# Kernel tuning notes

Hardware: AMD Instinct MI355X
Metric: run time of the kernel (lower is better)

The kernel has to match this reference:

```python
import jax, jax.numpy as jnp
import numpy as np

EMBED_DIM = 1024
NUM_HEADS = 16
D_K = EMBED_DIM // NUM_HEADS
B, T = 4, 2048


def setup_inputs() -> dict:
    key = jax.random.key(0)
    k_x, k_wqkv, k_wo = jax.random.split(key, 3)
    x = jax.random.normal(k_x, (B, T, EMBED_DIM), dtype=jnp.float32)
    # kaiming_normal on torch Linear weight [out,in]: std = sqrt(2/fan_in)=sqrt(2/embed_dim)
    std = np.sqrt(2.0 / EMBED_DIM).astype(np.float32)
    # store weights already transposed to [in, out] for y = x @ W + b
    W_qkv = jax.random.normal(k_wqkv, (EMBED_DIM, 3 * EMBED_DIM), dtype=jnp.float32) * std
    b_qkv = jnp.zeros((3 * EMBED_DIM,), dtype=jnp.float32)
    W_o = jax.random.normal(k_wo, (EMBED_DIM, EMBED_DIM), dtype=jnp.float32) * std
    b_o = jnp.zeros((EMBED_DIM,), dtype=jnp.float32)
    return {"x": x, "W_qkv": W_qkv, "b_qkv": b_qkv, "W_o": W_o, "b_o": b_o}


def reference(x, W_qkv, b_qkv, W_o, b_o):
    Bsz, Tlen, D = x.shape
    qkv = x @ W_qkv + b_qkv                      # [B,T,3D]
    q, k, v = jnp.split(qkv, 3, axis=-1)
    # split heads -> [B,H,T,d_k]
    def heads(t):
        return t.reshape(Bsz, Tlen, NUM_HEADS, D_K).transpose(0, 2, 1, 3)
    q, k, v = heads(q), heads(k), heads(v)
    scores = jnp.einsum('bhqd,bhkd->bhqk', q, k) / jnp.sqrt(jnp.float32(D_K))
    causal = jnp.tril(jnp.ones((Tlen, Tlen), dtype=bool))
    scores = jnp.where(causal[None, None], scores, -jnp.inf)
    attn = jax.nn.softmax(scores, axis=-1)
    out = jnp.einsum('bhqk,bhkd->bhqd', attn, v)  # [B,H,T,d_k]
    out = out.transpose(0, 2, 1, 3).reshape(Bsz, Tlen, D)
    return out @ W_o + b_o
```

## Files before the change

### kernel.cpp

```cpp
#include <hip/hip_runtime.h>
#include <hip/hip_bf16.h>
#include <math.h>

typedef unsigned short u16;
typedef __attribute__((ext_vector_type(8))) short bf16x8;
typedef __attribute__((ext_vector_type(4))) float f32x4;

#define BATCH 4
#define TSEQ  2048
#define HEADS 16
#define DK    64
#define EMB   1024
#define MROWS 8192
#define NQKV  3072
#define PHT   ((size_t)MROWS * EMB)

__device__ __forceinline__ u16 f2bf(float f) {
    union { float f; unsigned int i; } v;
    v.f = f;
    unsigned int x = v.i;
    return (u16)((x + 0x7FFFu + ((x >> 16) & 1u)) >> 16);
}

__device__ __forceinline__ unsigned int pk2bf(float a, float b) {
    float2 f2; f2.x = a; f2.y = b;
    union { __hip_bfloat162 h; unsigned int u; } cv;
    cv.h = __float22bfloat162_rn(f2);
    return cv.u;
}

__device__ __forceinline__ void gl2lds16(const u16* g, u16* l) {
    __builtin_amdgcn_global_load_lds(
        (const __attribute__((address_space(1))) unsigned int*)g,
        (__attribute__((address_space(3))) unsigned int*)l, 16, 0, 0);
}

__global__ __launch_bounds__(256) void convert_x(const float* __restrict__ X,
                                                 u16* __restrict__ Xb) {
    int i = (blockIdx.x * 256 + threadIdx.x) * 4;
    float4 v = *(const float4*)&X[i];
    ushort4 o;
    o.x = f2bf(v.x); o.y = f2bf(v.y); o.z = f2bf(v.z); o.w = f2bf(v.w);
    *(ushort4*)&Xb[i] = o;
}

__global__ __launch_bounds__(256) void transpose_both(const float* __restrict__ Wqkv,
                                                      const float* __restrict__ Wo,
                                                      u16* __restrict__ Wt,
                                                      u16* __restrict__ Wot) {
    __shared__ float tile[32][33];
    const int tx = threadIdx.x & 31, ty = threadIdx.x >> 5;
    const int K = 1024;
    const float* W;
    u16* D;
    int N, bx;
    if (blockIdx.x < 96) { W = Wqkv; D = Wt; N = 3072; bx = blockIdx.x; }
    else                 { W = Wo;   D = Wot; N = 1024; bx = blockIdx.x - 96; }
    const int by = blockIdx.y;
#pragma unroll
    for (int s = 0; s < 4; s++)
        tile[ty + 8 * s][tx] = W[(size_t)(by * 32 + ty + 8 * s) * N + bx * 32 + tx];
    __syncthreads();
#pragma unroll
    for (int s = 0; s < 4; s++)
        D[(size_t)(bx * 32 + ty + 8 * s) * K + by * 32 + tx] = f2bf(tile[tx][ty + 8 * s]);
}

template <int KDIM>
__device__ __forceinline__ void gemm_core256(const u16* __restrict__ A,
                                             const u16* __restrict__ Bt,
                                             u16* pool,
                                             int m0, int n0, int wm, int wn,
                                             int tid, int lo, int quad,
                                             f32x4 (&acc)[4][4]) {
    constexpr int NT = KDIM / 64;
    static_assert(NT >= 4 && (NT % 2) == 0, "NT even, >=4");

    const u16* ga[2];
    const u16* gb[4];
#pragma unroll
    for (int c = 0; c < 2; c++) {
        int chunk = c * 512 + tid, row = chunk >> 3, p = chunk & 7;
        ga[c] = A + (size_t)(m0 + row) * KDIM + (p ^ (row & 7)) * 8;
    }
#pragma unroll
    for (int c = 0; c < 4; c++) {
        int chunk = c * 512 + tid, row = chunk >> 3, p = chunk & 7;
        gb[c] = Bt + (size_t)(n0 + row) * KDIM + (p ^ (row & 7)) * 8;
    }

    auto stage = [&](int b) {
        u16* As = pool + b * 24576;
        u16* Bs = As + 8192;
#pragma unroll
        for (int c = 0; c < 2; c++) {
            gl2lds16(ga[c], As + (size_t)(c * 512 + tid) * 8);
            ga[c] += 64;
        }
#pragma unroll
        for (int c = 0; c < 4; c++) {
            gl2lds16(gb[c], Bs + (size_t)(c * 512 + tid) * 8);
            gb[c] += 64;
        }
    };

    bf16x8 afA[2][4], bwA[2][4], afB[2][4], bwB[2][4];

    auto ldfrag = [&](int b, bf16x8 (&af)[2][4], bf16x8 (&bw)[2][4]) {
        const u16* As = pool + b * 24576;
        const u16* Bs = As + 8192;
#pragma unroll
        for (int ks = 0; ks < 2; ks++) {
#pragma unroll
            for (int i = 0; i < 4; i++) {
                int r = wm + i * 16 + lo;
                af[ks][i] = *(const bf16x8*)&As[r * 64 + ((ks * 4 + quad) ^ (r & 7)) * 8];
            }
#pragma unroll
            for (int j = 0; j < 4; j++) {
                int r = wn + j * 16 + lo;
                bw[ks][j] = *(const bf16x8*)&Bs[r * 64 + ((ks * 4 + quad) ^ (r & 7)) * 8];
            }
        }
    };

    auto domfma = [&](bf16x8 (&af)[2][4], bf16x8 (&bw)[2][4]) {
        __builtin_amdgcn_sched_barrier(0);
        __builtin_amdgcn_s_setprio(1);
#pragma unroll
        for (int ks = 0; ks < 2; ks++)
#pragma unroll
            for (int i = 0; i < 4; i++)
#pragma unroll
                for (int j = 0; j < 4; j++)
                    acc[i][j] = __builtin_amdgcn_mfma_f32_16x16x32_bf16(
                        af[ks][i], bw[ks][j], acc[i][j], 0, 0, 0);
        __builtin_amdgcn_s_setprio(0);
    };

    stage(0); stage(1); stage(2);
    asm volatile("s_waitcnt vmcnt(12)" ::: "memory");
    __builtin_amdgcn_s_barrier();
    ldfrag(0, afA, bwA);

#pragma unroll
    for (int kt = 0; kt < NT; kt++) {
        if (kt < NT - 1) {
            asm volatile("s_waitcnt lgkmcnt(0)" ::: "memory");
            if (kt < NT - 2)
                asm volatile("s_waitcnt vmcnt(6)" ::: "memory");
            else
                asm volatile("s_waitcnt vmcnt(0)" ::: "memory");
            __builtin_amdgcn_s_barrier();
            if (kt + 3 < NT) stage(kt % 3);
            if (kt & 1) ldfrag((kt + 1) % 3, afA, bwA);
            else        ldfrag((kt + 1) % 3, afB, bwB);
        }
        if (kt & 1) domfma(afB, bwB);
        else        domfma(afA, bwA);
    }
}

__global__ __launch_bounds__(512, 1) void gemm1_mfma(const u16* __restrict__ A,
                                                     const u16* __restrict__ Bt,
                                                     const float* __restrict__ bias,
                                                     u16* __restrict__ qkv) {
    __shared__ u16 pool[3 * 24576];
    const int tid = threadIdx.x;
    const int lane = tid & 63, wv = tid >> 6;
    const int lo = lane & 15, quad = lane >> 4;
    const int gx = 12;
    int lin = blockIdx.y * gx + blockIdx.x;
    int swz = (lin & 7) * 96 + (lin >> 3);
    const int n0 = (swz % gx) * 256;
    const int m0 = (swz / gx) * 128;
    const int wm = (wv >> 2) * 64, wn = (wv & 3) * 64;
    const float scale2 = 0.18033688011112042f;
    f32x4 acc[4][4] = {};

    gemm_core256<1024>(A, Bt, pool, m0, n0, wm, wn, tid, lo, quad, acc);

    const int whichw = (n0 + wn) >> 10;
    if (whichw == 2) {
#pragma unroll
        for (int i = 0; i < 4; i++) {
            int mb = m0 + wm + i * 16 + quad * 4;
            int b = mb >> 11, t = mb & 2047;
#pragma unroll
            for (int j = 0; j < 4; j++) {
                int n = n0 + wn + j * 16 + lo;
                int rem = n & 1023;
                int h = rem >> 6, d = rem & 63;
                float bn = bias[n];
                ushort4 o;
                o.x = f2bf(acc[i][j][0] + bn);
                o.y = f2bf(acc[i][j][1] + bn);
                o.z = f2bf(acc[i][j][2] + bn);
                o.w = f2bf(acc[i][j][3] + bn);
                *(ushort4*)&qkv[2 * PHT +
                                (((size_t)(b * HEADS + h) * DK + d) * TSEQ + t)] = o;
            }
        }
    } else {
        const float sc = (whichw == 0) ? scale2 : 1.0f;
#pragma unroll
        for (int i = 0; i < 4; i++) {
#pragma unroll
            for (int r = 0; r < 4; r++) {
                int m = m0 + wm + i * 16 + quad * 4 + r;
                int b = m >> 11, t = m & 2047;
#pragma unroll
                for (int j = 0; j < 4; j++) {
                    int n = n0 + wn + j * 16 + lo;
                    float v = (acc[i][j][r] + bias[n]) * sc;
                    int rem = n & 1023;
                    int h = rem >> 6, d = rem & 63;
                    qkv[(size_t)whichw * PHT +
                        (((size_t)(b * HEADS + h) * TSEQ + t) * DK + d)] = f2bf(v);
                }
            }
        }
    }
}

__global__ __launch_bounds__(512, 1) void gemm2_mfma(const u16* __restrict__ A,
                                                     const u16* __restrict__ Bt,
                                                     const float* __restrict__ bias,
                                                     float* __restrict__ out) {
    __shared__ u16 pool[3 * 24576];
    const int tid = threadIdx.x;
    const int lane = tid & 63, wv = tid >> 6;
    const int lo = lane & 15, quad = lane >> 4;
    int lin = blockIdx.y * 4 + blockIdx.x;
    int swz = (lin & 7) * 32 + (lin >> 3);
    const int n0 = (swz & 3) * 256;
    const int m0 = (swz >> 2) * 128;
    const int wm = (wv >> 2) * 64, wn = (wv & 3) * 64;
    f32x4 acc[4][4] = {};

    gemm_core256<1024>(A, Bt, pool, m0, n0, wm, wn, tid, lo, quad, acc);

#pragma unroll
    for (int i = 0; i < 4; i++) {
#pragma unroll
        for (int r = 0; r < 4; r++) {
            int m = m0 + wm + i * 16 + quad * 4 + r;
#pragma unroll
            for (int j = 0; j < 4; j++) {
                int n = n0 + wn + j * 16 + lo;
                out[(size_t)m * EMB + n] = acc[i][j][r] + bias[n];
            }
        }
    }
}

__global__ __launch_bounds__(256, 2) void attn_mfma(const u16* __restrict__ Qg,
                                                    const u16* __restrict__ Kg,
                                                    const u16* __restrict__ Vg,
                                                    u16* __restrict__ AO) {
    __shared__ u16 pool[5 * 8192];
    u16* Rr = pool + 4 * 8192;

    const int tid = threadIdx.x;
    const int lane = tid & 63, wv = tid >> 6;
    const int lo = lane & 15, quad = lane >> 4;
    const int pair = blockIdx.x, bh = blockIdx.y;
    const size_t base = (size_t)bh * TSEQ * DK;
    const int b = bh >> 4, h = bh & 15;
    const bf16x8 onesf = {0x3F80, 0x3F80, 0x3F80, 0x3F80,
                          0x3F80, 0x3F80, 0x3F80, 0x3F80};

    auto stageKV = [&](int kt2, int bufsel) {
        u16* Kd = pool + bufsel * 8192;
        u16* Vd = pool + 2 * 8192 + bufsel * 8192;
#pragma unroll
        for (int c = 0; c < 4; c++) {
            int chunk = c * 256 + tid;
            int row = chunk >> 3, p = chunk & 7;
            int pg = p ^ (row & 7);
            gl2lds16(Kg + base + (size_t)(kt2 * 128 + row) * DK + pg * 8,
                     Kd + chunk * 8);
        }
#pragma unroll
        for (int c = 0; c < 4; c++) {
            int chunk = c * 256 + tid;
            int row = chunk >> 4, p = chunk & 15;
            int pg = p ^ (row & 15);
            gl2lds16(Vg + base + (size_t)row * TSEQ + kt2 * 128 + pg * 8,
                     Vd + chunk * 8);
        }
    };

    for (int qi = 0; qi < 2; qi++) {
        const int qt = qi ? (15 - pair) : pair;
        const int q0 = qt * 128;

        __syncthreads();
#pragma unroll
        for (int c = 0; c < 4; c++) {
            int chunk = c * 256 + tid;
            int row = chunk >> 3, p = chunk & 7;
            int pg = p ^ (row & 7);
            gl2lds16(Qg + base + (size_t)(q0 + row) * DK + pg * 8, Rr + chunk * 8);
        }
        stageKV(0, 0);
        __syncthreads();

        bf16x8 bq[2][2];
#pragma unroll
        for (int i = 0; i < 2; i++)
#pragma unroll
            for (int hh = 0; hh < 2; hh++) {
                int row = wv * 32 + i * 16 + lo;
                int ch = (hh * 4 + quad) ^ (row & 7);
                bq[i][hh] = *(const bf16x8*)&Rr[row * 64 + ch * 8];
            }

        f32x4 O[2][5] = {};

        for (int kt = 0; kt <= qt; kt++) {
            const int cur = kt & 1;
            if (kt) __syncthreads();
            if (kt < qt) stageKV(kt + 1, cur ^ 1);
            const u16* Ksc = pool + cur * 8192;
            const u16* Vtc = pool + 2 * 8192 + cur * 8192;

            const bool diag = (kt == qt);
            u16* Ps = Rr + wv * 2048;

#pragma unroll
            for (int jh = 0; jh < 2; jh++) {
                f32x4 st[4][2] = {};
#pragma unroll
                for (int hh = 0; hh < 2; hh++) {
#pragma unroll
                    for (int j2 = 0; j2 < 4; j2++) {
                        int row = (jh * 4 + j2) * 16 + lo;
                        int ch = (hh * 4 + quad) ^ (row & 7);
                        bf16x8 ak = *(const bf16x8*)&Ksc[row * 64 + ch * 8];
                        st[j2][0] = __builtin_amdgcn_mfma_f32_16x16x32_bf16(
                            ak, bq[0][hh], st[j2][0], 0, 0, 0);
                        st[j2][1] = __builtin_amdgcn_mfma_f32_16x16x32_bf16(
                            ak, bq[1][hh], st[j2][1], 0, 0, 0);
                    }
                }
#pragma unroll
                for (int j2 = 0; j2 < 4; j2++) {
#pragma unroll
                    for (int i = 0; i < 2; i++) {
                        float e[4];
#pragma unroll
                        for (int r = 0; r < 4; r++)
                            e[r] = __builtin_amdgcn_exp2f(st[j2][i][r]);
                        if (diag) {
                            int qr = q0 + wv * 32 + i * 16 + lo;
                            int kb = kt * 128 + (jh * 4 + j2) * 16 + quad * 4;
#pragma unroll
                            for (int r = 0; r < 4; r++)
                                if (kb + r > qr) e[r] = 0.f;
                        }
                        uint2 w;
                        w.x = pk2bf(e[0], e[1]);
                        w.y = pk2bf(e[2], e[3]);
                        int rowl = i * 16 + lo;
                        int chp = (2 * j2 + (quad >> 1)) ^ (lo & 7);
                        *(uint2*)&Ps[rowl * 64 + chp * 8 + (quad & 1) * 4] = w;
                    }
                }
#pragma unroll
                for (int hp = 0; hp < 2; hp++) {
                    bf16x8 ap[2], bv[4];
#pragma unroll
                    for (int i = 0; i < 2; i++) {
                        int rowl = i * 16 + lo;
                        int ch = (4 * hp + quad) ^ (lo & 7);
                        ap[i] = *(const bf16x8*)&Ps[rowl * 64 + ch * 8];
                    }
#pragma unroll
                    for (int jn = 0; jn < 4; jn++) {
                        int vrow = jn * 16 + lo;
                        int ch = (8 * jh + 4 * hp + quad) ^ (vrow & 15);
                        bv[jn] = *(const bf16x8*)&Vtc[vrow * 128 + ch * 8];
                    }
#pragma unroll
                    for (int i = 0; i < 2; i++) {
#pragma unroll
                        for (int jn = 0; jn < 4; jn++)
                            O[i][jn] = __builtin_amdgcn_mfma_f32_16x16x32_bf16(
                                ap[i], bv[jn], O[i][jn], 0, 0, 0);
                        O[i][4] = __builtin_amdgcn_mfma_f32_16x16x32_bf16(
                            ap[i], onesf, O[i][4], 0, 0, 0);
                    }
                }
            }
        }

#pragma unroll
        for (int i = 0; i < 2; i++)
#pragma unroll
            for (int r = 0; r < 4; r++) {
                int qrow = q0 + wv * 32 + i * 16 + quad * 4 + r;
                float inv = 1.f / O[i][4][r];
#pragma unroll
                for (int jn = 0; jn < 4; jn++) {
                    int d = jn * 16 + lo;
                    AO[(((size_t)b * TSEQ + qrow) * HEADS + h) * DK + d] =
                        f2bf(O[i][jn][r] * inv);
                }
            }
    }
}

extern "C" void kernel_launch(void* const* d_in, const int* in_sizes, int n_in,
                              void* d_out, int out_size, void* d_ws, size_t ws_size,
                              hipStream_t stream) {
    const float* x    = (const float*)d_in[0];
    const float* Wqkv = (const float*)d_in[1];
    const float* bqkv = (const float*)d_in[2];
    const float* Wo   = (const float*)d_in[3];
    const float* bo   = (const float*)d_in[4];
    float* out = (float*)d_out;

    u16* Xb  = (u16*)d_ws;
    u16* Wt  = Xb + PHT;
    u16* Wot = Wt + (size_t)NQKV * EMB;
    u16* qkv = Wot + (size_t)EMB * EMB;
    u16* AO  = Xb;

    convert_x<<<MROWS * EMB / 1024, 256, 0, stream>>>(x, Xb);
    transpose_both<<<dim3(96 + 32, 32), 256, 0, stream>>>(Wqkv, Wo, Wt, Wot);

    gemm1_mfma<<<dim3(NQKV / 256, MROWS / 128), 512, 0, stream>>>(Xb, Wt, bqkv, qkv);
    attn_mfma<<<dim3(8, BATCH * HEADS), 256, 0, stream>>>(
        qkv, qkv + PHT, qkv + 2 * PHT, AO);
    gemm2_mfma<<<dim3(EMB / 256, MROWS / 128), 512, 0, stream>>>(AO, Wot, bo, out);
}
```

Baseline: 226.9 us.

## Switch attention to 32x32x16 MFMA with register-resident P via permlane32 swap

Rewrites the attention inner loop to use 32x32x16 bf16 MFMA tiles instead of 16x16x32. The probability tile is repacked in registers with v_permlane32_swap rather than round-tripped through LDS. Q is now loaded directly from global into registers, which drops the Q staging buffer and shrinks LDS use. On diagonal tiles, key blocks that lie fully above the causal boundary for a wave are skipped. The cost is more accumulator registers per lane, which can lower occupancy.

Result: slower. 244.2 us (+7.6%).

```diff
diff --git a/kernel.cpp b/kernel.cpp
--- a/kernel.cpp
+++ b/kernel.cpp
@@ -5,6 +5,8 @@
 typedef unsigned short u16;
 typedef __attribute__((ext_vector_type(8))) short bf16x8;
 typedef __attribute__((ext_vector_type(4))) float f32x4;
+typedef __attribute__((ext_vector_type(16))) float f32x16;
+typedef __attribute__((ext_vector_type(4))) unsigned int u32x4;
 
 #define BATCH 4
 #define TSEQ  2048
@@ -258,12 +260,11 @@
                                                     const u16* __restrict__ Kg,
                                                     const u16* __restrict__ Vg,
                                                     u16* __restrict__ AO) {
-    __shared__ u16 pool[5 * 8192];
-    u16* Rr = pool + 4 * 8192;
+    __shared__ u16 pool[4 * 8192];
 
     const int tid = threadIdx.x;
     const int lane = tid & 63, wv = tid >> 6;
-    const int lo = lane & 15, quad = lane >> 4;
+    const int c = lane & 31, hf = lane >> 5;
     const int pair = blockIdx.x, bh = blockIdx.y;
     const size_t base = (size_t)bh * TSEQ * DK;
     const int b = bh >> 4, h = bh & 15;
@@ -274,16 +275,16 @@
         u16* Kd = pool + bufsel * 8192;
         u16* Vd = pool + 2 * 8192 + bufsel * 8192;
 #pragma unroll
-        for (int c = 0; c < 4; c++) {
-            int chunk = c * 256 + tid;
+        for (int cc = 0; cc < 4; cc++) {
+            int chunk = cc * 256 + tid;
             int row = chunk >> 3, p = chunk & 7;
             int pg = p ^ (row & 7);
             gl2lds16(Kg + base + (size_t)(kt2 * 128 + row) * DK + pg * 8,
                      Kd + chunk * 8);
         }
 #pragma unroll
-        for (int c = 0; c < 4; c++) {
-            int chunk = c * 256 + tid;
+        for (int cc = 0; cc < 4; cc++) {
+            int chunk = cc * 256 + tid;
             int row = chunk >> 4, p = chunk & 15;
             int pg = p ^ (row & 15);
             gl2lds16(Vg + base + (size_t)row * TSEQ + kt2 * 128 + pg * 8,
@@ -296,27 +297,15 @@
         const int q0 = qt * 128;
 
         __syncthreads();
-#pragma unroll
-        for (int c = 0; c < 4; c++) {
-            int chunk = c * 256 + tid;
-            int row = chunk >> 3, p = chunk & 7;
-            int pg = p ^ (row & 7);
-            gl2lds16(Qg + base + (size_t)(q0 + row) * DK + pg * 8, Rr + chunk * 8);
-        }
         stageKV(0, 0);
+        bf16x8 bq[4];
+#pragma unroll
+        for (int s = 0; s < 4; s++)
+            bq[s] = *(const bf16x8*)&Qg[base + (size_t)(q0 + wv * 32 + c) * DK +
+                                        s * 16 + hf * 8];
         __syncthreads();
 
-        bf16x8 bq[2][2];
-#pragma unroll
-        for (int i = 0; i < 2; i++)
-#pragma unroll
-            for (int hh = 0; hh < 2; hh++) {
-                int row = wv * 32 + i * 16 + lo;
-                int ch = (hh * 4 + quad) ^ (row & 7);
-                bq[i][hh] = *(const bf16x8*)&Rr[row * 64 + ch * 8];
-            }
-
-        f32x4 O[2][5] = {};
+        f32x16 O0 = {}, O1 = {}, ls = {};
 
         for (int kt = 0; kt <= qt; kt++) {
             const int cur = kt & 1;
@@ -324,90 +313,67 @@
             if (kt < qt) stageKV(kt + 1, cur ^ 1);
             const u16* Ksc = pool + cur * 8192;
             const u16* Vtc = pool + 2 * 8192 + cur * 8192;
-
             const bool diag = (kt == qt);
-            u16* Ps = Rr + wv * 2048;
-
-#pragma unroll
-            for (int jh = 0; jh < 2; jh++) {
-                f32x4 st[4][2] = {};
-#pragma unroll
-                for (int hh = 0; hh < 2; hh++) {
-#pragma unroll
-                    for (int j2 = 0; j2 < 4; j2++) {
-                        int row = (jh * 4 + j2) * 16 + lo;
-                        int ch = (hh * 4 + quad) ^ (row & 7);
-                        bf16x8 ak = *(const bf16x8*)&Ksc[row * 64 + ch * 8];
-                        st[j2][0] = __builtin_amdgcn_mfma_f32_16x16x32_bf16(
-                            ak, bq[0][hh], st[j2][0], 0, 0, 0);
-                        st[j2][1] = __builtin_amdgcn_mfma_f32_16x16x32_bf16(
-                            ak, bq[1][hh], st[j2][1], 0, 0, 0);
+
+#pragma unroll
+            for (int j = 0; j < 4; j++) {
+                if (!(diag && j > wv)) {
+                    f32x16 st = {};
+#pragma unroll
+                    for (int s = 0; s < 4; s++) {
+                        int row = j * 32 + c;
+                        bf16x8 ak = *(const bf16x8*)&Ksc[row * 64 +
+                                        (((s << 1) + hf) ^ (row & 7)) * 8];
+                        st = __builtin_amdgcn_mfma_f32_32x32x16_bf16(
+                            ak, bq[s], st, 0, 0, 0);
+                    }
+                    const bool part = diag && (j == wv);
+#pragma unroll
+                    for (int r = 0; r < 16; r++) {
+                        float e = __builtin_amdgcn_exp2f(st[r]);
+                        if (part) {
+                            int ko = (r & 3) + 8 * (r >> 2) + 4 * hf;
+                            if (ko > c) e = 0.f;
+                        }
+                        st[r] = e;
+                    }
+#pragma unroll
+                    for (int ks = 0; ks < 2; ks++) {
+                        const int br = ks * 8;
+                        unsigned int w0 = pk2bf(st[br + 0], st[br + 1]);
+                        unsigned int w1 = pk2bf(st[br + 2], st[br + 3]);
+                        unsigned int w2 = pk2bf(st[br + 4], st[br + 5]);
+                        unsigned int w3 = pk2bf(st[br + 6], st[br + 7]);
+                        asm volatile("v_permlane32_swap_b32 %0, %1"
+                                     : "+v"(w0), "+v"(w2));
+                        asm volatile("v_permlane32_swap_b32 %0, %1"
+                                     : "+v"(w1), "+v"(w3));
+                        union { u32x4 w; bf16x8 v; } pu;
+                        pu.w[0] = w0; pu.w[1] = w1; pu.w[2] = w2; pu.w[3] = w3;
+                        const int p0 = j * 4 + ks * 2 + hf;
+                        bf16x8 bv0 = *(const bf16x8*)&Vtc[c * 128 +
+                                        (p0 ^ (c & 15)) * 8];
+                        bf16x8 bv1 = *(const bf16x8*)&Vtc[(32 + c) * 128 +
+                                        (p0 ^ (c & 15)) * 8];
+                        O0 = __builtin_amdgcn_mfma_f32_32x32x16_bf16(
+                            pu.v, bv0, O0, 0, 0, 0);
+                        O1 = __builtin_amdgcn_mfma_f32_32x32x16_bf16(
+                            pu.v, bv1, O1, 0, 0, 0);
+                        ls = __builtin_amdgcn_mfma_f32_32x32x16_bf16(
+                            pu.v, onesf, ls, 0, 0, 0);
                     }
                 }
-#pragma unroll
-                for (int j2 = 0; j2 < 4; j2++) {
-#pragma unroll
-                    for (int i = 0; i < 2; i++) {
-                        float e[4];
-#pragma unroll
-                        for (int r = 0; r < 4; r++)
-                            e[r] = __builtin_amdgcn_exp2f(st[j2][i][r]);
-                        if (diag) {
-                            int qr = q0 + wv * 32 + i * 16 + lo;
-                            int kb = kt * 128 + (jh * 4 + j2) * 16 + quad * 4;
-#pragma unroll
-                            for (int r = 0; r < 4; r++)
-                                if (kb + r > qr) e[r] = 0.f;
-                        }
-                        uint2 w;
-                        w.x = pk2bf(e[0], e[1]);
-                        w.y = pk2bf(e[2], e[3]);
-                        int rowl = i * 16 + lo;
-                        int chp = (2 * j2 + (quad >> 1)) ^ (lo & 7);
-                        *(uint2*)&Ps[rowl * 64 + chp * 8 + (quad & 1) * 4] = w;
-                    }
-                }
-#pragma unroll
-                for (int hp = 0; hp < 2; hp++) {
-                    bf16x8 ap[2], bv[4];
-#pragma unroll
-                    for (int i = 0; i < 2; i++) {
-                        int rowl = i * 16 + lo;
-                        int ch = (4 * hp + quad) ^ (lo & 7);
-                        ap[i] = *(const bf16x8*)&Ps[rowl * 64 + ch * 8];
-                    }
-#pragma unroll
-                    for (int jn = 0; jn < 4; jn++) {
-                        int vrow = jn * 16 + lo;
-                        int ch = (8 * jh + 4 * hp + quad) ^ (vrow & 15);
-                        bv[jn] = *(const bf16x8*)&Vtc[vrow * 128 + ch * 8];
-                    }
-#pragma unroll
-                    for (int i = 0; i < 2; i++) {
-#pragma unroll
-                        for (int jn = 0; jn < 4; jn++)
-                            O[i][jn] = __builtin_amdgcn_mfma_f32_16x16x32_bf16(
-                                ap[i], bv[jn], O[i][jn], 0, 0, 0);
-                        O[i][4] = __builtin_amdgcn_mfma_f32_16x16x32_bf16(
-                            ap[i], onesf, O[i][4], 0, 0, 0);
-                    }
-                }
-            }
-        }
-
-#pragma unroll
-        for (int i = 0; i < 2; i++)
-#pragma unroll
-            for (int r = 0; r < 4; r++) {
-                int qrow = q0 + wv * 32 + i * 16 + quad * 4 + r;
-                float inv = 1.f / O[i][4][r];
-#pragma unroll
-                for (int jn = 0; jn < 4; jn++) {
-                    int d = jn * 16 + lo;
-                    AO[(((size_t)b * TSEQ + qrow) * HEADS + h) * DK + d] =
-                        f2bf(O[i][jn][r] * inv);
-                }
-            }
+            }
+        }
+
+#pragma unroll
+        for (int r = 0; r < 16; r++) {
+            int qrow = q0 + wv * 32 + (r & 3) + 8 * (r >> 2) + 4 * hf;
+            float inv = 1.f / ls[r];
+            size_t o = (((size_t)b * TSEQ + qrow) * HEADS + h) * DK;
+            AO[o + c]      = f2bf(O0[r] * inv);
+            AO[o + 32 + c] = f2bf(O1[r] * inv);
+        }
     }
 }
 
```
